# Performance work log

Measured on AMD Instinct MI355X. Metric: run time of the kernel, lower is better.

The kernel has to match this reference:

```python
import jax, jax.numpy as jnp
import numpy as np

H = 4          # attention heads
K = 16         # knn neighbors
EPS = 1e-5     # BatchNorm eps


def setup_inputs() -> dict:
    key = jax.random.key(0)
    ks = jax.random.split(key, 10)
    B, C, T, N = 2, 128, 32, 512
    OUT = 128
    HID = 2 * C + 2 * OUT  # ff hidden = in*2 + out*2
    s = 0.02
    return {
        "x_all": jax.random.normal(ks[0], (B, C, T, N), jnp.float32),
        "Wq": jax.random.normal(ks[1], (C, C), jnp.float32) * s,
        "Wk": jax.random.normal(ks[2], (C, C), jnp.float32) * s,
        "Wv": jax.random.normal(ks[3], (C, C), jnp.float32) * s,
        "W1": jax.random.normal(ks[4], (HID, C), jnp.float32) * s,
        "W2": jax.random.normal(ks[5], (OUT, HID), jnp.float32) * s,
        "bn_gamma": 1.0 + 0.1 * jax.random.normal(ks[6], (OUT,), jnp.float32),
        "bn_beta": 0.1 * jax.random.normal(ks[7], (OUT,), jnp.float32),
        "bn_mean": 0.1 * jax.random.normal(ks[8], (OUT,), jnp.float32),
        "bn_var": jax.random.uniform(ks[9], (OUT,), jnp.float32, 0.5, 1.5),
    }


def reference(x_all, Wq, Wk, Wv, W1, W2, bn_gamma, bn_beta, bn_mean, bn_var):
    B, C, T, N = x_all.shape
    D = C // H
    # --- st_group_points: candidate pool = 3 consecutive frames (replicate temporal pad), frame-major ---
    xp = jnp.concatenate([x_all[:, :, :1], x_all, x_all[:, :, -1:]], axis=2)   # (B,C,T+2,N)
    pool = jnp.stack([xp[:, :, :-2], xp[:, :, 1:-1], xp[:, :, 2:]], axis=3)    # (B,C,T,3,N)
    pool = pool.reshape(B, C, T, 3 * N)                                        # (B,C,T,3N)
    # KNN on xyz (channels 0:3); sqrt is monotone so topk on squared dists gives same indices
    a = x_all[:, :3]                                                           # (B,3,T,N)
    b = pool[:, :3]                                                            # (B,3,T,3N)
    d2 = jnp.sum((a[..., :, None] - b[..., None, :]) ** 2, axis=1)             # (B,T,N,3N)
    _, idx = jax.lax.top_k(-d2, K)                                             # (B,T,N,K) smallest-dist
    nb = jnp.take_along_axis(pool[:, :, :, None, :], idx[:, None], axis=-1)    # (B,C,T,N,K)
    rel = x_all[..., None] - nb                                                # diff grouping (B,C,T,N,K)
    # --- per-point local attention over K neighbors (1x1 convs == channel matmuls), all t at once ---
    q = jnp.einsum('oc,bctn->botn', Wq, x_all).reshape(B, H, D, T, N)
    k = jnp.einsum('oc,bctnk->botnk', Wk, rel).reshape(B, H, D, T, N, K)
    v = jnp.einsum('oc,bctnk->botnk', Wv, rel).reshape(B, H, D, T, N, K)
    energy = jnp.einsum('bhdtn,bhdtnk->bhtnk', q, k) / jnp.sqrt(jnp.float32(D))
    attn = jax.nn.softmax(energy, axis=-1)                                     # (B,H,T,N,K)
    agg = jnp.einsum('bhtnk,bhdtnk->bhdtn', attn, v).reshape(B, C, T, N)
    # --- residual + BatchNorm1d (eval mode, running stats) + conv feed-forward ---
    h = x_all + agg
    scale = (bn_gamma / jnp.sqrt(bn_var + EPS))[None, :, None, None]
    h = (h - bn_mean[None, :, None, None]) * scale + bn_beta[None, :, None, None]
    h = jax.nn.leaky_relu(jnp.einsum('oc,bctn->botn', W1, h), 0.2)
    y = jnp.einsum('oc,bctn->botn', W2, h)                                     # (B,OUT,T,N)
    return jnp.concatenate([x_all[:, :4], y], axis=1)                          # (B,4+OUT,T,N)
```

## Files before the change

### kernel.cpp

```cpp
#include <hip/hip_runtime.h>
#include <hip/hip_bf16.h>

typedef __hip_bfloat16 bf16;
typedef unsigned long long u64;
typedef __attribute__((ext_vector_type(8))) short short8;
typedef __attribute__((ext_vector_type(4))) float f32x4;

#define B_   2
#define C_   128
#define T_   32
#define N_   512
#define K_   16
#define HID_ 512
#define TN   (T_*N_)
#define PTS  (B_*T_*N_)

#define MFMA_BF16(a,b,c) __builtin_amdgcn_mfma_f32_16x16x32_bf16((a),(b),(c),0,0,0)

__device__ __forceinline__ float b2f(bf16 v){ return __bfloat162float(v); }
__device__ __forceinline__ bf16  f2b(float v){ return __float2bfloat16(v); }
__device__ __forceinline__ float bqf(short v){
  return __uint_as_float(((unsigned)(unsigned short)v) << 16);
}

__device__ __forceinline__ float ldc(const void* p, int i, bool f32) {
  return f32 ? ((const float*)p)[i] : b2f(((const bf16*)p)[i]);
}

__global__ __launch_bounds__(256) void convw_kernel(
    const void* __restrict__ x,
    const void* wq, const void* wk, const void* wv,
    const void* w1, const void* w2, const void* g, const void* bb,
    const void* m, const void* v,
    bf16* __restrict__ wqb, bf16* __restrict__ wkb, bf16* __restrict__ wvb,
    bf16* __restrict__ w1b, bf16* __restrict__ w2b,
    float* __restrict__ gf, float* __restrict__ bf_, float* __restrict__ mf,
    float* __restrict__ vf, int* __restrict__ flag)
{
  __shared__ int cnt;
  if (threadIdx.x == 0) cnt = 0;
  __syncthreads();
  const unsigned short* u = (const unsigned short*)x;
  int w = 0;
#pragma unroll
  for (int j = 0; j < 8; ++j) {
    unsigned short hv = u[threadIdx.x*8 + j];
    int e = (hv >> 7) & 0xFF;
    if (e >= 0x89) w++;
  }
  if (w) atomicAdd(&cnt, w);
  __syncthreads();
  bool f32 = (cnt > 32);
  if (blockIdx.x == 0 && threadIdx.x == 0) *flag = f32 ? 1 : 0;

  int i = blockIdx.x*256 + threadIdx.x;
  if (i < 16384) { wqb[i] = f2b(ldc(wq, i, f32)); return; } i -= 16384;
  if (i < 16384) { wkb[i] = f2b(ldc(wk, i, f32)); return; } i -= 16384;
  if (i < 16384) { wvb[i] = f2b(ldc(wv, i, f32)); return; } i -= 16384;
  if (i < 65536) { w1b[i] = f2b(ldc(w1, i, f32)); return; } i -= 65536;
  if (i < 65536) { w2b[i] = f2b(ldc(w2, i, f32)); return; } i -= 65536;
  if (i < 128)   { gf[i]  = ldc(g, i, f32); return; }       i -= 128;
  if (i < 128)   { bf_[i] = ldc(bb, i, f32); return; }      i -= 128;
  if (i < 128)   { mf[i]  = ldc(m, i, f32); return; }       i -= 128;
  if (i < 128)   { vf[i]  = ldc(v, i, f32); return; }
}

__device__ __forceinline__ u64 shflx64(u64 v, int m) {
  return (u64)__shfl_xor((long long)v, m, 64);
}

__device__ __forceinline__ void proj_gemm32(const bf16* __restrict__ W,
                                            bf16 (*ys)[136],
                                            const short8 am[2][4],
                                            int mrow, int quad, int ot)
{
  f32x4 acc[2];
#pragma unroll
  for (int mt=0;mt<2;++mt) acc[mt] = (f32x4){0.f,0.f,0.f,0.f};
#pragma unroll
  for (int kq=0;kq<4;++kq) {
    short8 bfr = *(const short8*)&W[(ot*16+mrow)*C_ + kq*32 + quad*8];
#pragma unroll
    for (int mt=0;mt<2;++mt) acc[mt] = MFMA_BF16(am[mt][kq], bfr, acc[mt]);
  }
#pragma unroll
  for (int mt=0;mt<2;++mt)
#pragma unroll
    for (int r=0;r<4;++r)
      ys[mt*16 + quad*4 + r][ot*16 + mrow] = f2b(acc[mt][r]);
}

__device__ __forceinline__ void tile_store32_512(bf16* __restrict__ dst,
                                                 const bf16 (*ys)[136], int tid)
{
  int flat = tid*8;
  int p = flat >> 7, c = flat & 127;
  *(short8*)&dst[(size_t)p*C_ + c] = *(const short8*)&ys[p][c];
}

__global__ __launch_bounds__(512) void projknn_kernel(
    const void* __restrict__ x, const int* __restrict__ flag,
    const bf16* __restrict__ wqb, const bf16* __restrict__ wkb, const bf16* __restrict__ wvb,
    bf16* __restrict__ xTb, bf16* QT, bf16* __restrict__ KT, bf16* __restrict__ VT,
    int* __restrict__ idxout)
{
  __shared__ __align__(16) char smem[28672];
  int tid = threadIdx.x;
  int blk = blockIdx.x;
  int g = blk / 5, r = blk - g*5;
  if (r == 4) {
    bf16 (*xs )[136] = (bf16(*)[136])(smem);
    bf16 (*ysK)[136] = (bf16(*)[136])(smem + 8704);
    bf16 (*ysV)[136] = (bf16(*)[136])(smem + 17408);
    int p0 = g * 32;
    int b = p0 >> 14; int tn0 = p0 & (TN-1);
    if (*flag) {
      const float* xbase = (const float*)x + (size_t)b*C_*TN + tn0;
#pragma unroll
      for (int it=0; it<8; ++it) {
        int i = it*512 + tid;
        int c = i >> 5, p = i & 31;
        xs[p][c] = f2b(xbase[(size_t)c*TN + p]);
      }
    } else {
      const bf16* xbase = (const bf16*)x + (size_t)b*C_*TN + tn0;
#pragma unroll
      for (int it=0; it<8; ++it) {
        int i = it*512 + tid;
        int c = i >> 5, p = i & 31;
        xs[p][c] = xbase[(size_t)c*TN + p];
      }
    }
    __syncthreads();
    tile_store32_512(xTb + (size_t)p0*C_, xs, tid);
    int lane = tid & 63, wave = tid >> 6;
    int mrow = lane & 15, quad = lane >> 4;
    short8 am[2][4];
#pragma unroll
    for (int mt=0;mt<2;++mt)
#pragma unroll
      for (int kq=0;kq<4;++kq)
        am[mt][kq] = *(const short8*)&xs[mt*16 + mrow][kq*32 + quad*8];
    __syncthreads();
    proj_gemm32(wqb, xs,  am, mrow, quad, wave);
    proj_gemm32(wkb, ysK, am, mrow, quad, wave);
    proj_gemm32(wvb, ysV, am, mrow, quad, wave);
    __syncthreads();
    tile_store32_512(QT + (size_t)p0*C_, xs,  tid);
    tile_store32_512(KT + (size_t)p0*C_, ysK, tid);
    tile_store32_512(VT + (size_t)p0*C_, ysV, tid);
  } else {
    float4* cand4 = (float4*)smem;
    u64 (*surv)[64] = (u64(*)[64])(smem + 24576);
    int kblk = g*4 + r;
    int row = kblk >> 6;
    int b = row >> 5, t = row & 31;
    int ng = kblk & 63;
    bool f32 = (*flag != 0);
#pragma unroll
    for (int q = 0; q < 3; ++q) {
      int tt = t - 1 + q; tt = tt < 0 ? 0 : (tt > T_-1 ? T_-1 : tt);
      size_t base = ((size_t)b*C_*T_ + tt)*(size_t)N_ + tid;
      float c0, c1, c2;
      if (f32) {
        const float* xp = (const float*)x;
        c0 = xp[base]; c1 = xp[base + (size_t)T_*N_]; c2 = xp[base + 2*(size_t)T_*N_];
      } else {
        const bf16* xp = (const bf16*)x;
        c0 = b2f(xp[base]); c1 = b2f(xp[base + (size_t)T_*N_]); c2 = b2f(xp[base + 2*(size_t)T_*N_]);
      }
      cand4[q*N_ + tid] = make_float4(c0, c1, c2, 0.f);
    }
    __syncthreads();
    int wave = tid >> 6, lane = tid & 63;
    int n = ng*8 + wave;
    float4 a = cand4[N_ + n];
    unsigned db[24];
#pragma unroll
    for (int j = 0; j < 24; ++j) {
      float4 cm = cand4[lane + (j << 6)];
      float dx = a.x - cm.x;
      float dy = a.y - cm.y;
      float dz = a.z - cm.z;
      float d2 = __fadd_rn(__fadd_rn(__fmul_rn(dx,dx), __fmul_rn(dy,dy)), __fmul_rn(dz,dz));
      db[j] = __float_as_uint(d2);
    }
    unsigned mm[12];
#pragma unroll
    for (int j = 0; j < 12; ++j) mm[j] = db[2*j] < db[2*j+1] ? db[2*j] : db[2*j+1];
#pragma unroll
    for (int j = 0; j < 6; ++j)  mm[j] = mm[2*j] < mm[2*j+1] ? mm[2*j] : mm[2*j+1];
#pragma unroll
    for (int j = 0; j < 3; ++j)  mm[j] = mm[2*j] < mm[2*j+1] ? mm[2*j] : mm[2*j+1];
    unsigned bd = mm[0] < mm[1] ? mm[0] : mm[1];
    bd = bd < mm[2] ? bd : mm[2];
    {
      unsigned lo = 0u, hi = 0x7f800000u;
#pragma unroll
      for (int it = 0; it < 16; ++it) {
        unsigned mid = lo + ((hi - lo) >> 1);
        int cge = __popcll(__ballot(bd <= mid));
        bool ge = (cge >= K_);
        hi = ge ? mid : hi;
        lo = ge ? lo : (mid + 1u);
      }
      bd = hi;
    }
    unsigned U = bd;
    int c = 0;
#pragma unroll
    for (int j = 0; j < 24; ++j) c += (db[j] <= U) ? 1 : 0;
    int ofs = 0, total = 0;
#pragma unroll
    for (int bit = 0; bit < 5; ++bit) {
      u64 mball = __ballot(((c >> bit) & 1) != 0);
      unsigned below = __builtin_amdgcn_mbcnt_hi((unsigned)(mball >> 32),
                        __builtin_amdgcn_mbcnt_lo((unsigned)mball, 0u));
      ofs   += ((int)below) << bit;
      total += (__popcll(mball)) << bit;
    }
    int point = (b*T_ + t)*N_ + n;
    if (total <= 64) {
#pragma unroll
      for (int j = 0; j < 24; ++j) {
        if (db[j] <= U) {
          surv[wave][ofs] = ((u64)db[j] << 11) | (unsigned)(lane + (j << 6));
          ++ofs;
        }
      }
      if (lane == total) surv[wave][lane] = ~0ull;
      __threadfence_block();
      u64 kk = (lane < total) ? surv[wave][lane] : ~0ull;
      int npair = (total + 1) >> 1;
      int rank = 0;
      const ulonglong2* sk2 = (const ulonglong2*)&surv[wave][0];
#pragma unroll 4
      for (int i2 = 0; i2 < npair; ++i2) {
        ulonglong2 kp = sk2[i2];
        rank += (kp.x < kk) ? 1 : 0;
        rank += (kp.y < kk) ? 1 : 0;
      }
      if (rank < K_) idxout[point*K_ + rank] = (int)(kk & 2047u);
    } else {
      u64 key[24];
#pragma unroll
      for (int j = 0; j < 24; ++j)
        key[j] = ((u64)db[j] << 32) | (unsigned)(lane + (j << 6));
      u64 res = ~0ull;
#pragma unroll 1
      for (int rr = 0; rr < 16; ++rr) {
        u64 m2 = key[0];
#pragma unroll
        for (int j = 1; j < 24; ++j) m2 = (key[j] < m2) ? key[j] : m2;
#pragma unroll
        for (int s = 32; s >= 1; s >>= 1) {
          u64 p = shflx64(m2, s);
          m2 = (p < m2) ? p : m2;
        }
        if (lane == rr) res = m2;
        int mwin = (int)(m2 & 0xffffffffu);
        int sel = ((mwin & 63) == lane) ? (mwin >> 6) : -1;
#pragma unroll
        for (int j = 0; j < 24; ++j) if (j == sel) key[j] = ~0ull;
      }
      if (lane < K_) idxout[point*K_ + lane] = (int)(res & 0xffffffffu);
    }
  }
}

__global__ __launch_bounds__(256) void attnmlp_kernel(
    const int* __restrict__ idxin, const bf16* __restrict__ xTb,
    const bf16* __restrict__ QT, const bf16* __restrict__ KT,
    const bf16* __restrict__ VT,
    const float* __restrict__ gf, const float* __restrict__ bf_,
    const float* __restrict__ mf, const float* __restrict__ vf,
    const bf16* __restrict__ w1b, const bf16* __restrict__ w2b,
    const void* __restrict__ x, const int* __restrict__ flag,
    void* __restrict__ out)
{
  __shared__ __align__(16) char smem[25600];
  bf16  (*hTl)[136]      = (bf16 (*)[136])     (smem);
  float (*qbuf)[C_]      = (float(*)[C_])      (smem + 8704);
  int   (*col_lds)[K_]   = (int  (*)[K_])      (smem + 9728);
  float (*e_lds)[4][K_]  = (float(*)[4][K_])   (smem + 9856);
  bf16  (*vbuf)[K_][136] = (bf16 (*)[K_][136]) (smem + 10368);
  bf16  (*hidh)[264]     = (bf16 (*)[264])     (smem + 8704);

  int tid = threadIdx.x;
  int gblk = (blockIdx.x & 7)*128 + (blockIdx.x >> 3);
  int p0 = gblk * 32;
  int bb = p0 >> 14;
  int tn0 = p0 & (TN-1);
  bool f32o = (*flag != 0);
  if (tid < 128) {
    int c = tid >> 5, p = tid & 31;
    size_t si = ((size_t)bb*C_ + c)*TN + tn0 + p;
    size_t di = ((size_t)bb*132 + c)*TN + tn0 + p;
    if (f32o) ((float*)out)[di] = ((const float*)x)[si];
    else      ((bf16*)out)[di]  = ((const bf16*)x)[si];
  }

  int pt = tid >> 7, o = tid & 127;
  float sc = gf[o] / sqrtf(vf[o] + 1e-5f);
  float smean = mf[o], sbeta = bf_[o];
  float vselfC, xselfC;
  {
    int point = p0 + pt;
    int b = point >> 14, tn = point & (TN-1), t = tn >> 9;
    if (o < K_) {
      int m = idxin[point*K_ + o];
      int j = m >> 9, nn = m & (N_-1);
      int tt = t-1+j; tt = tt<0?0:(tt>T_-1?T_-1:tt);
      col_lds[pt][o] = ((b*T_ + tt)*N_ + nn)*C_;
    }
    int self = point*C_;
    vselfC = b2f(VT[self + o]);
    xselfC = b2f(xTb[self + o]);
    qbuf[pt][o] = b2f(QT[self + o]);
  }
  __syncthreads();
#pragma unroll 1
  for (int sub = 0; sub < 16; ++sub) {
    {
      int k = o >> 3, c = o & 7, hd = c >> 1;
      int src = col_lds[pt][k] + c*16;
      short8 kv0 = *(const short8*)&KT[src];
      short8 kv1 = *(const short8*)&KT[src + 8];
      short8 vv0 = *(const short8*)&VT[src];
      short8 vv1 = *(const short8*)&VT[src + 8];
      *(short8*)&vbuf[pt][k][c*16]     = vv0;
      *(short8*)&vbuf[pt][k][c*16 + 8] = vv1;
      const float* qp = &qbuf[pt][c*16];
      float qv[16];
      *(float4*)&qv[0]  = *(const float4*)(qp);
      *(float4*)&qv[4]  = *(const float4*)(qp + 4);
      *(float4*)&qv[8]  = *(const float4*)(qp + 8);
      *(float4*)&qv[12] = *(const float4*)(qp + 12);
      float e = 0.f;
#pragma unroll
      for (int i2=0;i2<8;++i2) e = fmaf(qv[i2],   bqf(kv0[i2]), e);
#pragma unroll
      for (int i2=0;i2<8;++i2) e = fmaf(qv[8+i2], bqf(kv1[i2]), e);
      e += __shfl_xor(e, 1, 64);
      if (!(c & 1)) e_lds[pt][hd][k] = -e * 0.17677669529663687f;
    }
    __syncthreads();
    {
      int hd = o >> 5;
      float e[16]; float mx = -3e38f;
#pragma unroll
      for (int k=0;k<K_;++k){ e[k]=e_lds[pt][hd][k]; mx=fmaxf(mx,e[k]); }
      float ssum=0.f;
#pragma unroll
      for (int k=0;k<K_;++k){ e[k]=__expf(e[k]-mx); ssum+=e[k]; }
      float inv = 1.f/ssum;
      float acc = vselfC;
#pragma unroll
      for (int k=0;k<K_;++k)
        acc = fmaf(-(e[k]*inv), b2f(vbuf[pt][k][o]), acc);
      float hv = xselfC + acc;
      hTl[sub*2 + pt][o] = f2b((hv - smean)*sc + sbeta);
    }
    if (sub < 15) {
      int point = p0 + (sub+1)*2 + pt;
      int b = point >> 14, tn = point & (TN-1), t = tn >> 9;
      if (o < K_) {
        int m = idxin[point*K_ + o];
        int j = m >> 9, nn = m & (N_-1);
        int tt = t-1+j; tt = tt<0?0:(tt>T_-1?T_-1:tt);
        col_lds[pt][o] = ((b*T_ + tt)*N_ + nn)*C_;
      }
      int self = point*C_;
      vselfC = b2f(VT[self + o]);
      xselfC = b2f(xTb[self + o]);
      qbuf[pt][o] = b2f(QT[self + o]);
    }
    __syncthreads();
  }

  int lane = tid & 63, wave = tid >> 6;
  int mrow = lane & 15, quad = lane >> 4;
  f32x4 acc2[2][2];
#pragma unroll
  for (int oi=0;oi<2;++oi)
#pragma unroll
    for (int mt=0;mt<2;++mt) acc2[oi][mt] = (f32x4){0.f,0.f,0.f,0.f};

#pragma unroll
  for (int half = 0; half < 2; ++half) {
    if (half) __syncthreads();
    short8 am[2][4];
#pragma unroll
    for (int mt=0;mt<2;++mt)
#pragma unroll
      for (int kq=0;kq<4;++kq)
        am[mt][kq] = *(const short8*)&hTl[mt*16 + mrow][kq*32 + quad*8];
#pragma unroll
    for (int oi = 0; oi < 4; ++oi) {
      int ot_g = half*16 + wave*4 + oi;
      int otl  = wave*4 + oi;
      f32x4 acc[2];
#pragma unroll
      for (int mt=0;mt<2;++mt) acc[mt] = (f32x4){0.f,0.f,0.f,0.f};
#pragma unroll
      for (int kq=0;kq<4;++kq) {
        short8 bfr = *(const short8*)&w1b[(ot_g*16+mrow)*C_ + kq*32 + quad*8];
#pragma unroll
        for (int mt=0;mt<2;++mt) acc[mt] = MFMA_BF16(am[mt][kq], bfr, acc[mt]);
      }
#pragma unroll
      for (int mt=0;mt<2;++mt)
#pragma unroll
        for (int r=0;r<4;++r) {
          float z = acc[mt][r];
          hidh[mt*16 + quad*4 + r][otl*16 + mrow] = f2b(z > 0.f ? z : 0.2f*z);
        }
    }
    __syncthreads();
#pragma unroll
    for (int kc = 0; kc < 4; ++kc) {
      short8 ha[2][2];
#pragma unroll
      for (int mt=0;mt<2;++mt)
#pragma unroll
        for (int kk=0;kk<2;++kk)
          ha[mt][kk] = *(const short8*)&hidh[mt*16 + mrow][(kc*2+kk)*32 + quad*8];
#pragma unroll
      for (int oi=0;oi<2;++oi) {
        int ot2 = wave*2 + oi;
#pragma unroll
        for (int kk=0;kk<2;++kk) {
          int ks_g = half*8 + kc*2 + kk;
          short8 bfr = *(const short8*)&w2b[(ot2*16+mrow)*HID_ + ks_g*32 + quad*8];
#pragma unroll
          for (int mt=0;mt<2;++mt)
            acc2[oi][mt] = MFMA_BF16(ha[mt][kk], bfr, acc2[oi][mt]);
        }
      }
    }
  }
  size_t obase = (size_t)bb*132*TN;
#pragma unroll
  for (int oi=0;oi<2;++oi) {
    int ch = (wave*2+oi)*16 + mrow;
#pragma unroll
    for (int mt=0;mt<2;++mt) {
      int tn = tn0 + mt*16 + quad*4;
      size_t oidx = obase + (size_t)(4+ch)*TN + tn;
      if (f32o) {
        *(f32x4*)&((float*)out)[oidx] = acc2[oi][mt];
      } else {
        bf16 tmp[4];
#pragma unroll
        for (int r=0;r<4;++r) tmp[r] = f2b(acc2[oi][mt][r]);
        *(u64*)&((bf16*)out)[oidx] = *(u64*)tmp;
      }
    }
  }
}

extern "C" void kernel_launch(void* const* d_in, const int* in_sizes, int n_in,
                              void* d_out, int out_size, void* d_ws, size_t ws_size,
                              hipStream_t stream)
{
  (void)in_sizes; (void)n_in; (void)out_size; (void)ws_size;
  const void* x = d_in[0];
  char* ws = (char*)d_ws;
  const size_t MB = (size_t)1<<20;
  bf16*  QT  = (bf16* )(ws + 0*MB);
  bf16*  KT  = (bf16* )(ws + 8*MB);
  bf16*  VT  = (bf16* )(ws + 16*MB);
  bf16*  xTb = (bf16* )(ws + 24*MB);
  int*   idxw= (int*  )(ws + 32*MB);
  bf16*  wqb = (bf16* )(ws + 34*MB);
  bf16*  wkb = (bf16* )(ws + 34*MB + 0x8000);
  bf16*  wvb = (bf16* )(ws + 34*MB + 0x10000);
  bf16*  w1b = (bf16* )(ws + 34*MB + 0x18000);
  bf16*  w2b = (bf16* )(ws + 34*MB + 0x38000);
  float* gf  = (float*)(ws + 34*MB + 0x58000);
  float* bf_ = (float*)(ws + 34*MB + 0x58200);
  float* mf  = (float*)(ws + 34*MB + 0x58400);
  float* vf  = (float*)(ws + 34*MB + 0x58600);
  int*  flag = (int*  )(ws + 34*MB + 0x58800);

  convw_kernel  <<<dim3(706), dim3(256), 0, stream>>>(
      x, d_in[1], d_in[2], d_in[3], d_in[4], d_in[5],
      d_in[6], d_in[7], d_in[8], d_in[9],
      wqb, wkb, wvb, w1b, w2b, gf, bf_, mf, vf, flag);
  projknn_kernel<<<dim3(5120), dim3(512), 0, stream>>>(
      x, flag, wqb, wkb, wvb, xTb, QT, KT, VT, idxw);
  attnmlp_kernel<<<dim3(PTS/32), dim3(256), 0, stream>>>(
      idxw, xTb, QT, KT, VT, gf, bf_, mf, vf, w1b, w2b, x, flag, d_out);
}
```

Before: 198.6 us.

## Prefetch next sub-block's neighbor K/V gathers into registers during current compute

Computes all 32 points' neighbor column offsets up front into a shared table instead of per-iteration index loads. Issues the gathered K/V and self Q/V/x loads for the next pair of points right after the energy step, into registers and a double-buffered q buffer, so global latency overlaps the softmax and aggregation of the current pair. This costs extra registers and shared memory for the prefetch buffers.

```diff
diff --git a/kernel.cpp b/kernel.cpp
--- a/kernel.cpp
+++ b/kernel.cpp
@@ -279,12 +279,12 @@
     void* __restrict__ out)
 {
   __shared__ __align__(16) char smem[25600];
-  bf16  (*hTl)[136]      = (bf16 (*)[136])     (smem);
-  float (*qbuf)[C_]      = (float(*)[C_])      (smem + 8704);
-  int   (*col_lds)[K_]   = (int  (*)[K_])      (smem + 9728);
-  float (*e_lds)[4][K_]  = (float(*)[4][K_])   (smem + 9856);
-  bf16  (*vbuf)[K_][136] = (bf16 (*)[K_][136]) (smem + 10368);
-  bf16  (*hidh)[264]     = (bf16 (*)[264])     (smem + 8704);
+  bf16  (*hTl)[136]       = (bf16 (*)[136])      (smem);
+  int   (*colbuf)[K_]     = (int  (*)[K_])       (smem + 8704);
+  float (*qbuf)[2][C_]    = (float(*)[2][C_])    (smem + 10752);
+  float (*e_lds)[4][K_]   = (float(*)[4][K_])    (smem + 12800);
+  bf16  (*vbuf)[K_][136]  = (bf16 (*)[K_][136])  (smem + 13312);
+  bf16  (*hidh)[264]      = (bf16 (*)[264])      (smem + 8704);
 
   int tid = threadIdx.x;
   int gblk = (blockIdx.x & 7)*128 + (blockIdx.x >> 3);
@@ -300,37 +300,44 @@
     else      ((bf16*)out)[di]  = ((const bf16*)x)[si];
   }
 
+  int tblk = tn0 >> 9;
+#pragma unroll
+  for (int it = 0; it < 2; ++it) {
+    int e = it*256 + tid;
+    int row = e >> 4, kk = e & 15;
+    int m = idxin[(p0 + row)*K_ + kk];
+    int j = m >> 9, nn = m & (N_-1);
+    int tt = tblk-1+j; tt = tt<0?0:(tt>T_-1?T_-1:tt);
+    colbuf[row][kk] = ((bb*T_ + tt)*N_ + nn)*C_;
+  }
+
   int pt = tid >> 7, o = tid & 127;
+  int k = o >> 3, c = o & 7, hd = c >> 1;
   float sc = gf[o] / sqrtf(vf[o] + 1e-5f);
   float smean = mf[o], sbeta = bf_[o];
-  float vselfC, xselfC;
+  float vselfC, xselfC, vselfN = 0.f, xselfN = 0.f;
   {
-    int point = p0 + pt;
-    int b = point >> 14, tn = point & (TN-1), t = tn >> 9;
-    if (o < K_) {
-      int m = idxin[point*K_ + o];
-      int j = m >> 9, nn = m & (N_-1);
-      int tt = t-1+j; tt = tt<0?0:(tt>T_-1?T_-1:tt);
-      col_lds[pt][o] = ((b*T_ + tt)*N_ + nn)*C_;
-    }
-    int self = point*C_;
+    int self = (p0 + pt)*C_;
     vselfC = b2f(VT[self + o]);
     xselfC = b2f(xTb[self + o]);
-    qbuf[pt][o] = b2f(QT[self + o]);
+    qbuf[0][pt][o] = b2f(QT[self + o]);
   }
   __syncthreads();
+  short8 kv0, kv1, vv0, vv1;
+  {
+    int src = colbuf[pt][k] + c*16;
+    kv0 = *(const short8*)&KT[src];
+    kv1 = *(const short8*)&KT[src + 8];
+    vv0 = *(const short8*)&VT[src];
+    vv1 = *(const short8*)&VT[src + 8];
+  }
 #pragma unroll 1
   for (int sub = 0; sub < 16; ++sub) {
+    int cur = sub & 1, nxt = cur ^ 1;
     {
-      int k = o >> 3, c = o & 7, hd = c >> 1;
-      int src = col_lds[pt][k] + c*16;
-      short8 kv0 = *(const short8*)&KT[src];
-      short8 kv1 = *(const short8*)&KT[src + 8];
-      short8 vv0 = *(const short8*)&VT[src];
-      short8 vv1 = *(const short8*)&VT[src + 8];
       *(short8*)&vbuf[pt][k][c*16]     = vv0;
       *(short8*)&vbuf[pt][k][c*16 + 8] = vv1;
-      const float* qp = &qbuf[pt][c*16];
+      const float* qp = &qbuf[cur][pt][c*16];
       float qv[16];
       *(float4*)&qv[0]  = *(const float4*)(qp);
       *(float4*)&qv[4]  = *(const float4*)(qp + 4);
@@ -344,37 +351,36 @@
       e += __shfl_xor(e, 1, 64);
       if (!(c & 1)) e_lds[pt][hd][k] = -e * 0.17677669529663687f;
     }
+    if (sub < 15) {
+      int row = (sub+1)*2 + pt;
+      int src = colbuf[row][k] + c*16;
+      kv0 = *(const short8*)&KT[src];
+      kv1 = *(const short8*)&KT[src + 8];
+      vv0 = *(const short8*)&VT[src];
+      vv1 = *(const short8*)&VT[src + 8];
+      int self = (p0 + row)*C_;
+      vselfN = b2f(VT[self + o]);
+      xselfN = b2f(xTb[self + o]);
+      qbuf[nxt][pt][o] = b2f(QT[self + o]);
+    }
     __syncthreads();
     {
-      int hd = o >> 5;
-      float e[16]; float mx = -3e38f;
-#pragma unroll
-      for (int k=0;k<K_;++k){ e[k]=e_lds[pt][hd][k]; mx=fmaxf(mx,e[k]); }
+      int hd2 = o >> 5;
+      float ee[16]; float mx = -3e38f;
+#pragma unroll
+      for (int kk=0;kk<K_;++kk){ ee[kk]=e_lds[pt][hd2][kk]; mx=fmaxf(mx,ee[kk]); }
       float ssum=0.f;
 #pragma unroll
-      for (int k=0;k<K_;++k){ e[k]=__expf(e[k]-mx); ssum+=e[k]; }
+      for (int kk=0;kk<K_;++kk){ ee[kk]=__expf(ee[kk]-mx); ssum+=ee[kk]; }
       float inv = 1.f/ssum;
       float acc = vselfC;
 #pragma unroll
-      for (int k=0;k<K_;++k)
-        acc = fmaf(-(e[k]*inv), b2f(vbuf[pt][k][o]), acc);
+      for (int kk=0;kk<K_;++kk)
+        acc = fmaf(-(ee[kk]*inv), b2f(vbuf[pt][kk][o]), acc);
       float hv = xselfC + acc;
       hTl[sub*2 + pt][o] = f2b((hv - smean)*sc + sbeta);
     }
-    if (sub < 15) {
-      int point = p0 + (sub+1)*2 + pt;
-      int b = point >> 14, tn = point & (TN-1), t = tn >> 9;
-      if (o < K_) {
-        int m = idxin[point*K_ + o];
-        int j = m >> 9, nn = m & (N_-1);
-        int tt = t-1+j; tt = tt<0?0:(tt>T_-1?T_-1:tt);
-        col_lds[pt][o] = ((b*T_ + tt)*N_ + nn)*C_;
-      }
-      int self = point*C_;
-      vselfC = b2f(VT[self + o]);
-      xselfC = b2f(xTb[self + o]);
-      qbuf[pt][o] = b2f(QT[self + o]);
-    }
+    vselfC = vselfN; xselfC = xselfN;
     __syncthreads();
   }
 
```

New measurement: 190.1 us. 4.3% less time.
